# Kernel tuning notes

Measured on AMD Instinct MI355X. Metric: run time of the kernel, lower is better.

## Reference

```python
import jax, jax.numpy as jnp
import numpy as np

D_MODEL = 1024
N_HEADS = 16
D_FF = 4096
EPS = 1e-5


def setup_inputs() -> dict:
    key = jax.random.key(0)
    ks = jax.random.split(key, 13)
    d, f = D_MODEL, D_FF
    s = 1.0 / np.sqrt(d)
    sf = 1.0 / np.sqrt(f)
    return {
        "x": jax.random.normal(ks[0], (2, 2048, d), dtype=jnp.float32),
        "Wq": jax.random.normal(ks[1], (d, d), dtype=jnp.float32) * s,
        "bq": jnp.zeros((d,), jnp.float32),
        "Wk": jax.random.normal(ks[2], (d, d), dtype=jnp.float32) * s,
        "bk": jnp.zeros((d,), jnp.float32),
        "Wv": jax.random.normal(ks[3], (d, d), dtype=jnp.float32) * s,
        "bv": jnp.zeros((d,), jnp.float32),
        "Wo": jax.random.normal(ks[4], (d, d), dtype=jnp.float32) * s,
        "bo": jnp.zeros((d,), jnp.float32),
        "W1": jax.random.normal(ks[5], (f, d), dtype=jnp.float32) * s,
        "b1": jnp.zeros((f,), jnp.float32),
        "W2": jax.random.normal(ks[6], (d, f), dtype=jnp.float32) * sf,
        "b2": jnp.zeros((d,), jnp.float32),
        "g1": jnp.ones((d,), jnp.float32),
        "be1": jnp.zeros((d,), jnp.float32),
        "g2": jnp.ones((d,), jnp.float32),
        "be2": jnp.zeros((d,), jnp.float32),
    }


def _layernorm(x, g, b):
    mu = jnp.mean(x, axis=-1, keepdims=True)
    var = jnp.mean(jnp.square(x - mu), axis=-1, keepdims=True)
    return (x - mu) * jax.lax.rsqrt(var + EPS) * g + b


def reference(x, Wq, bq, Wk, bk, Wv, bv, Wo, bo, W1, b1, W2, b2, g1, be1, g2, be2):
    B, S, D = x.shape
    H = N_HEADS
    dk = D // H
    # QKV projections (torch Linear: x @ W.T + b), reshape to [B,H,S,dk]
    def proj(W, b):
        return (x @ W.T + b).reshape(B, S, H, dk).transpose(0, 2, 1, 3)
    Q, K, V = proj(Wq, bq), proj(Wk, bk), proj(Wv, bv)
    scores = jnp.einsum("bhsd,bhtd->bhst", Q, K) / jnp.sqrt(jnp.float32(dk))
    attn = jax.nn.softmax(scores, axis=-1)
    ctx = jnp.einsum("bhst,bhtd->bhsd", attn, V)
    ctx = ctx.transpose(0, 2, 1, 3).reshape(B, S, D)
    attn_out = ctx @ Wo.T + bo
    x1 = _layernorm(x + attn_out, g1, be1)
    ff = jax.nn.relu(x1 @ W1.T + b1) @ W2.T + b2
    return _layernorm(x1 + ff, g2, be2)
```

## Files before the change

kernel.cpp:

```cpp
#include <hip/hip_runtime.h>

typedef unsigned short u16;
typedef unsigned int u32;
typedef unsigned long long u64;
typedef __attribute__((ext_vector_type(8))) short short8;
typedef __attribute__((ext_vector_type(4))) float f32x4;

#define D_MODEL 1024
#define SEQ 2048
#define NH 16
#define DK 64
#define DFF 4096
#define NTOK 4096
#define LOG2E 1.44269504f

__device__ __forceinline__ u16 f2bf(float f) {
    unsigned x = __builtin_bit_cast(unsigned, f);
    x = x + 0x7fffu + ((x >> 16) & 1u);
    return (u16)(x >> 16);
}

__device__ __forceinline__ float fexp2(float x) {
    float r;
    asm("v_exp_f32 %0, %1" : "=v"(r) : "v"(x));
    return r;
}

__device__ __forceinline__ void gload_lds16(const void* g, void* l) {
    __builtin_amdgcn_global_load_lds(
        (__attribute__((address_space(1))) void*)g,
        (__attribute__((address_space(3))) void*)l, 16, 0, 0);
}

__device__ __forceinline__ void cvt_body(const float* __restrict__ in,
                                         u16* __restrict__ out, int blk) {
    size_t i = ((size_t)blk * 256 + threadIdx.x) * 4;
    float4 v = *(const float4*)(in + i);
    out[i + 0] = f2bf(v.x);
    out[i + 1] = f2bf(v.y);
    out[i + 2] = f2bf(v.z);
    out[i + 3] = f2bf(v.w);
}

__global__ __launch_bounds__(256) void cvt_bf16_x4(
    const float* __restrict__ sx, const float* __restrict__ s0,
    const float* __restrict__ s1, const float* __restrict__ s2,
    const float* __restrict__ s3, u16* __restrict__ dx, u16* __restrict__ d0,
    u16* __restrict__ d1, u16* __restrict__ d2, u16* __restrict__ d3) {
    int f = blockIdx.x;
    if (f < 4096) {
        cvt_body(sx, dx, f);
    } else {
        int which = (f - 4096) >> 10, blk = (f - 4096) & 1023;
        const float* s = which == 0 ? s0 : which == 1 ? s1 : which == 2 ? s2 : s3;
        u16* d = which == 0 ? d0 : which == 1 ? d1 : which == 2 ? d2 : d3;
        cvt_body(s, d, blk);
    }
}

__global__ __launch_bounds__(256) void cvt_bf16_2(
    const float* __restrict__ s0, const float* __restrict__ s1,
    u16* __restrict__ d0, u16* __restrict__ d1) {
    int which = blockIdx.x >> 12, blk = blockIdx.x & 4095;
    cvt_body(which ? s1 : s0, which ? d1 : d0, blk);
}

template <int BM, int BN>
__device__ __forceinline__ void gemm_acc(const u16* __restrict__ A,
                                         const u16* __restrict__ W,
                                         int K, int m0, int n0,
                                         f32x4 (&acc)[BM / 32][BN / 32]) {
    constexpr int MR = BM / 32, NR = BN / 32;
    __shared__ short8 As[2][BM / 2][8];
    __shared__ short8 Bs[2][BN / 2][8];
    const int tid = threadIdx.x;
    const int lane = tid & 63, w = tid >> 6;
    const int l15 = lane & 15, lg = lane >> 4;
    const int wr = (w >> 1) * (BM / 2), wc = (w & 1) * (BN / 2);
    const int pswA = l15 >> 1;
    const int cbase = ((l15 & 1) << 2) + lg;

#pragma unroll
    for (int i = 0; i < MR; ++i)
#pragma unroll
        for (int j = 0; j < NR; ++j) acc[i][j] = (f32x4){0.f, 0.f, 0.f, 0.f};

#define STAGE_AB(B_, K0)                                                       \
    {                                                                          \
        _Pragma("unroll") for (int j = 0; j < BM / 64; ++j) {                  \
            int idx = j * 256 + tid;                                           \
            int prow = idx >> 3;                                               \
            int s = (idx & 7) ^ (prow & 7);                                    \
            int lrow = prow * 2 + (s >> 2), lc = s & 3;                        \
            gload_lds16(A + (size_t)(m0 + lrow) * K + (K0) + lc * 8,           \
                        (char*)As[B_] + (j * 256 + w * 64) * 16);              \
        }                                                                      \
        _Pragma("unroll") for (int j = 0; j < BN / 64; ++j) {                  \
            int idx = j * 256 + tid;                                           \
            int prow = idx >> 3;                                               \
            int s = (idx & 7) ^ (prow & 7);                                    \
            int lrow = prow * 2 + (s >> 2), lc = s & 3;                        \
            gload_lds16(W + (size_t)(n0 + lrow) * K + (K0) + lc * 8,           \
                        (char*)Bs[B_] + (j * 256 + w * 64) * 16);              \
        }                                                                      \
    }
#define COMPUTE(B_)                                                            \
    {                                                                          \
        short8 af[MR], bf[NR];                                                 \
        _Pragma("unroll") for (int m = 0; m < MR; ++m)                         \
            af[m] = As[B_][(wr + m * 16) / 2 + (l15 >> 1)][cbase ^ pswA];      \
        _Pragma("unroll") for (int n = 0; n < NR; ++n)                         \
            bf[n] = Bs[B_][(wc + n * 16) / 2 + (l15 >> 1)][cbase ^ pswA];      \
        _Pragma("unroll") for (int m = 0; m < MR; ++m)                         \
            _Pragma("unroll") for (int n = 0; n < NR; ++n)                     \
                acc[m][n] = __builtin_amdgcn_mfma_f32_16x16x32_bf16(           \
                    af[m], bf[n], acc[m][n], 0, 0, 0);                         \
    }

    STAGE_AB(0, 0);
    for (int k0 = 0; k0 < K; k0 += 64) {
        __syncthreads();
        STAGE_AB(1, k0 + 32);
        COMPUTE(0);
        __syncthreads();
        if (k0 + 64 < K) STAGE_AB(0, k0 + 64);
        COMPUTE(1);
    }
#undef STAGE_AB
#undef COMPUTE
}

template <int BM, int BN, int EPI, int XCD>
__global__ __launch_bounds__(256) void gemm_bt(
    const u16* __restrict__ A, const u16* __restrict__ W,
    const float* __restrict__ bias, u16* __restrict__ outb,
    float* __restrict__ outf, int M, int N, int K) {
    int m0, n0;
    if (XCD) {
        int f = blockIdx.x;
        int xcd = f & 7, j = f >> 3;
        int mq = xcd >> 1, nh = xcd & 1;
        int mi = j & 7, ni = j >> 3;
        m0 = (mq * 8 + mi) * BM;
        n0 = (nh * 16 + ni) * BN;
    } else {
        m0 = blockIdx.y * BM;
        n0 = blockIdx.x * BN;
    }
    f32x4 acc[BM / 32][BN / 32];
    gemm_acc<BM, BN>(A, W, K, m0, n0, acc);
    const int lane = threadIdx.x & 63, w = threadIdx.x >> 6;
    const int l15 = lane & 15, lg = lane >> 4;
    const int wr = (w >> 1) * (BM / 2), wc = (w & 1) * (BN / 2);
#pragma unroll
    for (int m = 0; m < BM / 32; ++m)
#pragma unroll
        for (int n = 0; n < BN / 32; ++n) {
            int gn = n0 + wc + n * 16 + l15;
            float bv = bias[gn];
#pragma unroll
            for (int r = 0; r < 4; ++r) {
                int gm = m0 + wr + m * 16 + lg * 4 + r;
                float v = acc[m][n][r] + bv;
                if (EPI == 0) outf[(size_t)gm * N + gn] = v;
                else outb[(size_t)gm * N + gn] = f2bf(fmaxf(v, 0.f));
            }
        }
}

__global__ __launch_bounds__(256) void gemm_k64(
    const u16* __restrict__ A, const u16* __restrict__ W,
    const float* __restrict__ bias, float* __restrict__ outf,
    float* __restrict__ outf2, int M, int N, int K, int KZ) {
    __shared__ short8 As[64][8];
    __shared__ short8 Bs[128][8];
    const int tid = threadIdx.x;
    const int lane = tid & 63, w = tid >> 6;
    const int l15 = lane & 15, lg = lane >> 4;
    const int wr = (w >> 1) * 32, wc = (w & 1) * 64;
    const int psw = l15 & 7;
    const int f = blockIdx.x;
    const int xcd = f & 7, j = f >> 3;
    const int mi = j & 7, n = (j >> 3) & 7, kz = j >> 6;
    const int m0 = (xcd * 8 + mi) * 64, n0 = n * 128;
    const int kl = K / KZ, kbase = kz * kl;
    float* out = kz ? outf2 : outf;

    f32x4 acc[2][4];
#pragma unroll
    for (int i = 0; i < 2; ++i)
#pragma unroll
        for (int jj = 0; jj < 4; ++jj) acc[i][jj] = (f32x4){0.f, 0.f, 0.f, 0.f};

    for (int k0 = kbase; k0 < kbase + kl; k0 += 64) {
        __syncthreads();
#pragma unroll
        for (int jj = 0; jj < 2; ++jj) {
            int idx = jj * 256 + tid;
            int r = idx >> 3, ck = idx & 7;
            gload_lds16(A + (size_t)(m0 + r) * K + k0 + ((ck ^ (r & 7)) * 8),
                        (char*)As + (jj * 256 + w * 64) * 16);
        }
#pragma unroll
        for (int jj = 0; jj < 4; ++jj) {
            int idx = jj * 256 + tid;
            int r = idx >> 3, ck = idx & 7;
            gload_lds16(W + (size_t)(n0 + r) * K + k0 + ((ck ^ (r & 7)) * 8),
                        (char*)Bs + (jj * 256 + w * 64) * 16);
        }
        __syncthreads();

#pragma unroll
        for (int kk = 0; kk < 2; ++kk) {
            short8 af[2], bf[4];
#pragma unroll
            for (int m = 0; m < 2; ++m)
                af[m] = As[wr + m * 16 + l15][(kk * 4 + lg) ^ psw];
#pragma unroll
            for (int nn = 0; nn < 4; ++nn)
                bf[nn] = Bs[wc + nn * 16 + l15][(kk * 4 + lg) ^ psw];
#pragma unroll
            for (int m = 0; m < 2; ++m)
#pragma unroll
                for (int nn = 0; nn < 4; ++nn)
                    acc[m][nn] = __builtin_amdgcn_mfma_f32_16x16x32_bf16(
                        af[m], bf[nn], acc[m][nn], 0, 0, 0);
        }
    }

#pragma unroll
    for (int m = 0; m < 2; ++m)
#pragma unroll
        for (int nn = 0; nn < 4; ++nn) {
            int gn = n0 + wc + nn * 16 + l15;
            float bv = (kz == 0) ? bias[gn] : 0.f;
#pragma unroll
            for (int r = 0; r < 4; ++r) {
                int gm = m0 + wr + m * 16 + lg * 4 + r;
                out[(size_t)gm * N + gn] = acc[m][nn][r] + bv;
            }
        }
}

__global__ __launch_bounds__(256) void gemm_qkv(
    const u16* __restrict__ A, const u16* __restrict__ Wq,
    const u16* __restrict__ Wk, const u16* __restrict__ Wv,
    const float* __restrict__ bq, const float* __restrict__ bk,
    const float* __restrict__ bv, u16* __restrict__ Qo, u16* __restrict__ Ko,
    u16* __restrict__ Vo) {
    const int f = blockIdx.x;
    const int xcd = f & 7, j = f >> 3;
    const int mi = j & 3, q = j >> 2;
    const int mat = q >> 3;
    const int m0 = (xcd * 4 + mi) * 128, n0 = (q & 7) * 128;
    const u16* W = mat == 0 ? Wq : (mat == 1 ? Wk : Wv);
    const float* bias = mat == 0 ? bq : (mat == 1 ? bk : bv);
    const float scale = (mat == 0) ? 0.125f * LOG2E : 1.0f;
    f32x4 acc[4][4];
    gemm_acc<128, 128>(A, W, D_MODEL, m0, n0, acc);
    const int lane = threadIdx.x & 63, w = threadIdx.x >> 6;
    const int l15 = lane & 15, lg = lane >> 4;
    const int wr = (w >> 1) * 64, wc = (w & 1) * 64;

    if (mat == 2) {
#pragma unroll
        for (int m = 0; m < 4; ++m)
#pragma unroll
            for (int n = 0; n < 4; ++n) {
                int gn = n0 + wc + n * 16 + l15;
                float bv2 = bias[gn];
                int h = gn >> 6, d = gn & 63;
                int gm0 = m0 + wr + m * 16 + lg * 4;
                int b = gm0 >> 11, s = gm0 & 2047;
                u64 pk = (u64)f2bf(acc[m][n][0] + bv2) |
                         ((u64)f2bf(acc[m][n][1] + bv2) << 16) |
                         ((u64)f2bf(acc[m][n][2] + bv2) << 32) |
                         ((u64)f2bf(acc[m][n][3] + bv2) << 48);
                size_t obase = (size_t)(b * NH + h) * DK * SEQ;
                int soff = (s & ~63) + ((((s >> 3) & 7) ^ (d & 7)) << 3) + (s & 7);
                *(u64*)(Vo + obase + (size_t)d * SEQ + soff) = pk;
            }
    } else {
        u16* out = mat == 0 ? Qo : Ko;
#pragma unroll
        for (int m = 0; m < 4; ++m)
#pragma unroll
            for (int n = 0; n < 4; ++n) {
                int gn = n0 + wc + n * 16 + l15;
                float bv2 = bias[gn];
                int h = gn >> 6, d = gn & 63;
#pragma unroll
                for (int r = 0; r < 4; ++r) {
                    int gm = m0 + wr + m * 16 + lg * 4 + r;
                    int b = gm >> 11, s = gm & 2047;
                    float v = (acc[m][n][r] + bv2) * scale;
                    out[(((size_t)(b * NH + h)) * SEQ + s) * DK + d] = f2bf(v);
                }
            }
    }
}

#define KVB 64
__global__ __launch_bounds__(256) void attn_fwd(const u16* __restrict__ Q,
                                                const u16* __restrict__ Kp,
                                                const u16* __restrict__ Vg_,
                                                u16* __restrict__ ctx) {
    __shared__ __align__(16) u16 Kt[2][64 * 64];
    __shared__ __align__(16) u16 Vt[2][64 * 64];
    __shared__ __align__(16) u16 Ps[4][16 * 64];

    const int tid = threadIdx.x;
    const int lane = tid & 63;
    const int w = tid >> 6;
    const int l15 = lane & 15;
    const int lg = lane >> 4;
    const int f = blockIdx.x + 32 * blockIdx.y;
    const int bh = f & 31;
    const int qblk = f >> 5;
    const int qbase = qblk * 64 + w * 16;
    const u16* Qb = Q + (size_t)bh * SEQ * DK;
    const u16* Kb = Kp + (size_t)bh * SEQ * DK;
    const u16* Vg = Vg_ + (size_t)bh * DK * SEQ;

    short8 qf[2];
#pragma unroll
    for (int hf = 0; hf < 2; ++hf)
        qf[hf] = *(const short8*)(Qb + (size_t)(qbase + l15) * DK + hf * 32 + lg * 8);

    short8 onesf;
#pragma unroll
    for (int e = 0; e < 8; ++e) onesf[e] = (short)0x3F80;

    f32x4 zero = {0.f, 0.f, 0.f, 0.f};
    f32x4 o[4], o1 = zero;
#pragma unroll
    for (int db = 0; db < 4; ++db) o[db] = zero;
    float m_own = 0.f;

    u16* Pu = Ps[w];
    const int psw = l15 & 7;

#define STAGE_V(T0, BUF)                                                       \
    {                                                                          \
        _Pragma("unroll") for (int j = 0; j < 2; ++j) {                        \
            int idx = j * 256 + tid;                                           \
            gload_lds16(Vg + (size_t)(idx >> 3) * SEQ + (T0) + (idx & 7) * 8,  \
                        (char*)Vt[BUF] + (j * 256 + w * 64) * 16);             \
        }                                                                      \
    }
#define STAGE_K(T0, BUF)                                                       \
    {                                                                          \
        _Pragma("unroll") for (int j = 0; j < 2; ++j) {                        \
            int idx = j * 256 + tid;                                           \
            int kv = idx >> 3, ck = idx & 7;                                   \
            gload_lds16(Kb + (size_t)((T0) + kv) * DK + ((ck ^ (kv & 7)) * 8), \
                        (char*)Kt[BUF] + (j * 256 + w * 64) * 16);             \
        }                                                                      \
    }
#define KF(BUF, NB, HALF)                                                      \
    (*(const short8*)((const char*)Kt[BUF] + ((NB)*16 + l15) * 128 +           \
                      (((((HALF)*4 + lg)) ^ psw) << 4)))

#define ATTN_TILE(BUF)                                                         \
    {                                                                          \
        f32x4 seed = {-m_own, -m_own, -m_own, -m_own};                         \
        f32x4 sc[4];                                                           \
        __builtin_amdgcn_s_setprio(1);                                         \
        _Pragma("unroll") for (int nb = 0; nb < 4; ++nb) {                     \
            sc[nb] = __builtin_amdgcn_mfma_f32_16x16x32_bf16(                  \
                KF(BUF, nb, 0), qf[0], seed, 0, 0, 0);                         \
            sc[nb] = __builtin_amdgcn_mfma_f32_16x16x32_bf16(                  \
                KF(BUF, nb, 1), qf[1], sc[nb], 0, 0, 0);                       \
        }                                                                      \
        __builtin_amdgcn_s_setprio(0);                                         \
        float a0 = fmaxf(fmaxf(sc[0][0], sc[0][1]), sc[0][2]);                 \
        float a1 = fmaxf(fmaxf(sc[0][3], sc[1][0]), sc[1][1]);                 \
        float a2 = fmaxf(fmaxf(sc[1][2], sc[1][3]), sc[2][0]);                 \
        float a3 = fmaxf(fmaxf(sc[2][1], sc[2][2]), sc[2][3]);                 \
        float a4 = fmaxf(fmaxf(sc[3][0], sc[3][1]), sc[3][2]);                 \
        float lm = fmaxf(fmaxf(fmaxf(a0, a1), a2),                             \
                         fmaxf(fmaxf(a3, a4), sc[3][3]));                      \
        if (__any(lm > 8.f)) {                                                 \
            float rv = fmaxf(lm, __shfl_xor(lm, 16));                          \
            rv = fmaxf(rv, __shfl_xor(rv, 32));                                \
            float rvp = fmaxf(rv, 0.f);                                        \
            float fac = fexp2(-rvp);                                           \
            m_own += rvp;                                                      \
            _Pragma("unroll") for (int nb = 0; nb < 4; ++nb)                   \
                _Pragma("unroll") for (int r = 0; r < 4; ++r)                  \
                    sc[nb][r] -= rvp;                                          \
            _Pragma("unroll") for (int r = 0; r < 4; ++r) {                    \
                float fr = __shfl(fac, lg * 4 + r);                            \
                o1[r] *= fr;                                                   \
                _Pragma("unroll") for (int db = 0; db < 4; ++db)               \
                    o[db][r] *= fr;                                            \
            }                                                                  \
        }                                                                      \
        _Pragma("unroll") for (int nb = 0; nb < 4; ++nb) {                     \
            float p0 = fexp2(sc[nb][0]);                                       \
            float p1 = fexp2(sc[nb][1]);                                       \
            float p2 = fexp2(sc[nb][2]);                                       \
            float p3 = fexp2(sc[nb][3]);                                       \
            u32 pk01 = __builtin_amdgcn_perm(__builtin_bit_cast(u32, p1),      \
                                             __builtin_bit_cast(u32, p0),      \
                                             0x07060302u);                     \
            u32 pk23 = __builtin_amdgcn_perm(__builtin_bit_cast(u32, p3),      \
                                             __builtin_bit_cast(u32, p2),      \
                                             0x07060302u);                     \
            int ck = (nb * 2 + (lg >> 1)) ^ psw;                               \
            u64* dst = (u64*)(Pu + l15 * 64 + ck * 8 + (lg & 1) * 4);          \
            *dst = (u64)pk01 | ((u64)pk23 << 32);                              \
        }                                                                      \
        short8 pa[2];                                                          \
        _Pragma("unroll") for (int ts = 0; ts < 2; ++ts)                       \
            pa[ts] = *(const short8*)(Pu + l15 * 64 + (((ts * 4 + lg) ^ psw) * 8)); \
        __builtin_amdgcn_s_setprio(1);                                         \
        _Pragma("unroll") for (int db = 0; db < 4; ++db) {                     \
            const int d = db * 16 + l15;                                       \
            _Pragma("unroll") for (int ts = 0; ts < 2; ++ts) {                 \
                short8 vb = *(const short8*)((const char*)Vt[BUF] + d * 128 +  \
                                             (((ts * 4 + lg) ^ psw) << 4));    \
                o[db] = __builtin_amdgcn_mfma_f32_16x16x32_bf16(               \
                    pa[ts], vb, o[db], 0, 0, 0);                               \
            }                                                                  \
        }                                                                      \
        o1 = __builtin_amdgcn_mfma_f32_16x16x32_bf16(pa[0], onesf, o1, 0, 0, 0); \
        o1 = __builtin_amdgcn_mfma_f32_16x16x32_bf16(pa[1], onesf, o1, 0, 0, 0); \
        __builtin_amdgcn_s_setprio(0);                                         \
    }

    STAGE_K(0, 0);
    STAGE_V(0, 0);

    for (int t0 = 0; t0 < SEQ; t0 += 2 * KVB) {
        __syncthreads();
        STAGE_K(t0 + KVB, 1);
        STAGE_V(t0 + KVB, 1);
        ATTN_TILE(0);
        __syncthreads();
        if (t0 + 2 * KVB < SEQ) {
            STAGE_K(t0 + 2 * KVB, 0);
            STAGE_V(t0 + 2 * KVB, 0);
        }
        ATTN_TILE(1);
    }

    const int b = bh >> 4, h = bh & 15;
#pragma unroll
    for (int r = 0; r < 4; ++r) {
        float inv = 1.0f / o1[r];
        int srow = qbase + lg * 4 + r;
        size_t rowoff = ((size_t)(b * SEQ + srow)) * D_MODEL + h * DK;
#pragma unroll
        for (int db = 0; db < 4; ++db)
            ctx[rowoff + db * 16 + l15] = f2bf(o[db][r] * inv);
    }
#undef STAGE_V
#undef STAGE_K
#undef KF
#undef ATTN_TILE
}

__global__ __launch_bounds__(256) void ln_res(const float* __restrict__ X,
                                              const float* __restrict__ Y,
                                              const float* __restrict__ Y2,
                                              const float* __restrict__ gamma,
                                              const float* __restrict__ beta,
                                              float* __restrict__ outf,
                                              u16* __restrict__ outb) {
    __shared__ float red[8];
    const int row = blockIdx.x, t = threadIdx.x;
    const size_t off = (size_t)row * D_MODEL + t * 4;
    float4 xv = *(const float4*)(X + off);
    float4 yv = *(const float4*)(Y + off);
    float sx = xv.x + yv.x, sy = xv.y + yv.y, sz = xv.z + yv.z, sw = xv.w + yv.w;
    if (Y2) {
        float4 y2 = *(const float4*)(Y2 + off);
        sx += y2.x; sy += y2.y; sz += y2.z; sw += y2.w;
    }
    float ps = sx + sy + sz + sw;
#pragma unroll
    for (int o2 = 32; o2; o2 >>= 1) ps += __shfl_xor(ps, o2);
    if ((t & 63) == 0) red[t >> 6] = ps;
    __syncthreads();
    float mu = (red[0] + red[1] + red[2] + red[3]) * (1.0f / D_MODEL);
    float d0 = sx - mu, d1 = sy - mu, d2 = sz - mu, d3 = sw - mu;
    float p2 = d0 * d0 + d1 * d1 + d2 * d2 + d3 * d3;
#pragma unroll
    for (int o2 = 32; o2; o2 >>= 1) p2 += __shfl_xor(p2, o2);
    if ((t & 63) == 0) red[4 + (t >> 6)] = p2;
    __syncthreads();
    float var = (red[4] + red[5] + red[6] + red[7]) * (1.0f / D_MODEL);
    float rstd = rsqrtf(var + 1e-5f);
    float4 gv = *(const float4*)(gamma + t * 4);
    float4 bv = *(const float4*)(beta + t * 4);
    float r0 = d0 * rstd * gv.x + bv.x;
    float r1 = d1 * rstd * gv.y + bv.y;
    float r2 = d2 * rstd * gv.z + bv.z;
    float r3 = d3 * rstd * gv.w + bv.w;
    float4 res; res.x = r0; res.y = r1; res.z = r2; res.w = r3;
    *(float4*)(outf + off) = res;
    if (outb) {
        outb[off + 0] = f2bf(r0);
        outb[off + 1] = f2bf(r1);
        outb[off + 2] = f2bf(r2);
        outb[off + 3] = f2bf(r3);
    }
}

extern "C" void kernel_launch(void* const* d_in, const int* in_sizes, int n_in,
                              void* d_out, int out_size, void* d_ws, size_t ws_size,
                              hipStream_t stream) {
    (void)in_sizes; (void)n_in; (void)out_size; (void)ws_size;
    const float* x  = (const float*)d_in[0];
    const float* Wq = (const float*)d_in[1];
    const float* bq = (const float*)d_in[2];
    const float* Wk = (const float*)d_in[3];
    const float* bk = (const float*)d_in[4];
    const float* Wv = (const float*)d_in[5];
    const float* bv = (const float*)d_in[6];
    const float* Wo = (const float*)d_in[7];
    const float* bo = (const float*)d_in[8];
    const float* W1 = (const float*)d_in[9];
    const float* b1 = (const float*)d_in[10];
    const float* W2 = (const float*)d_in[11];
    const float* b2 = (const float*)d_in[12];
    const float* g1 = (const float*)d_in[13];
    const float* be1 = (const float*)d_in[14];
    const float* g2 = (const float*)d_in[15];
    const float* be2 = (const float*)d_in[16];

    char* ws = (char*)d_ws;
    u16* xb   = (u16*)(ws);
    u16* Qb   = (u16*)(ws + ((size_t)8 << 20));
    u16* Kb   = (u16*)(ws + ((size_t)16 << 20));
    u16* Vb   = (u16*)(ws + ((size_t)24 << 20));
    float* x1 = (float*)(ws + ((size_t)32 << 20));
    float* Fs = (float*)(ws + ((size_t)48 << 20));
    u16* hb   = (u16*)(ws + ((size_t)64 << 20));
    u16* Wqb = hb;
    u16* Wkb = hb + (1u << 20);
    u16* Wvb = hb + (2u << 20);
    u16* Wob = hb + (3u << 20);
    u16* W1b = Qb;
    u16* W2b = Kb;
    u16* Vtg = (u16*)Fs;
    u16* ctxb = xb;
    u16* x1b  = Vb;
    float* Fs2 = (float*)ws;

    cvt_bf16_x4<<<dim3(8192), 256, 0, stream>>>(x, Wq, Wk, Wv, Wo,
                                                xb, Wqb, Wkb, Wvb, Wob);

    gemm_qkv<<<dim3(768), 256, 0, stream>>>(xb, Wqb, Wkb, Wvb, bq, bk, bv,
                                            Qb, Kb, Vtg);

    attn_fwd<<<dim3(SEQ / 64, 32), 256, 0, stream>>>(Qb, Kb, Vtg, ctxb);

    cvt_bf16_2<<<dim3(8192), 256, 0, stream>>>(W1, W2, W1b, W2b);

    gemm_k64<<<dim3(512), 256, 0, stream>>>(ctxb, Wob, bo, Fs, nullptr,
                                            NTOK, D_MODEL, D_MODEL, 1);

    ln_res<<<dim3(NTOK), 256, 0, stream>>>(x, Fs, nullptr, g1, be1, x1, x1b);

    gemm_bt<128, 128, 1, 1><<<dim3(1024), 256, 0, stream>>>(
        x1b, W1b, b1, hb, nullptr, NTOK, DFF, D_MODEL);

    gemm_k64<<<dim3(1024), 256, 0, stream>>>(hb, W2b, b2, Fs, Fs2,
                                             NTOK, D_MODEL, DFF, 2);

    ln_res<<<dim3(NTOK), 256, 0, stream>>>(x1, Fs, Fs2, g2, be2,
                                           (float*)d_out, nullptr);
}
```

Measured before the change: 274.1 us.

## Store GEMM outputs as bf16 and widen attention blocks to 128 queries

The Wo and W2 GEMM epilogues now write bf16 instead of fp32 partial results, and the residual-LayerNorm kernels read them as bf16. This halves the write and read traffic for those intermediates, at the cost of extra rounding before the LayerNorm. The attention kernel now uses 512 threads (8 waves) per block covering 128 query rows, so each staged K/V tile is shared by twice as many waves. Each thread now issues one staging load instead of two.

Result: faster. 255.4 us (-6.8%).

```diff
diff --git a/kernel.cpp b/kernel.cpp
--- a/kernel.cpp
+++ b/kernel.cpp
@@ -18,6 +18,10 @@
     unsigned x = __builtin_bit_cast(unsigned, f);
     x = x + 0x7fffu + ((x >> 16) & 1u);
     return (u16)(x >> 16);
+}
+
+__device__ __forceinline__ float bf2f(u16 v) {
+    return __builtin_bit_cast(float, (u32)v << 16);
 }
 
 __device__ __forceinline__ float fexp2(float x) {
@@ -170,8 +174,8 @@
 
 __global__ __launch_bounds__(256) void gemm_k64(
     const u16* __restrict__ A, const u16* __restrict__ W,
-    const float* __restrict__ bias, float* __restrict__ outf,
-    float* __restrict__ outf2, int M, int N, int K, int KZ) {
+    const float* __restrict__ bias, u16* __restrict__ outb,
+    u16* __restrict__ outb2, int M, int N, int K, int KZ) {
     __shared__ short8 As[64][8];
     __shared__ short8 Bs[128][8];
     const int tid = threadIdx.x;
@@ -184,7 +188,7 @@
     const int mi = j & 7, n = (j >> 3) & 7, kz = j >> 6;
     const int m0 = (xcd * 8 + mi) * 64, n0 = n * 128;
     const int kl = K / KZ, kbase = kz * kl;
-    float* out = kz ? outf2 : outf;
+    u16* out = kz ? outb2 : outb;
 
     f32x4 acc[2][4];
 #pragma unroll
@@ -237,7 +241,7 @@
 #pragma unroll
             for (int r = 0; r < 4; ++r) {
                 int gm = m0 + wr + m * 16 + lg * 4 + r;
-                out[(size_t)gm * N + gn] = acc[m][nn][r] + bv;
+                out[(size_t)gm * N + gn] = f2bf(acc[m][nn][r] + bv);
             }
         }
 }
@@ -301,23 +305,23 @@
 }
 
 #define KVB 64
-__global__ __launch_bounds__(256) void attn_fwd(const u16* __restrict__ Q,
+__global__ __launch_bounds__(512) void attn_fwd(const u16* __restrict__ Q,
                                                 const u16* __restrict__ Kp,
                                                 const u16* __restrict__ Vg_,
                                                 u16* __restrict__ ctx) {
     __shared__ __align__(16) u16 Kt[2][64 * 64];
     __shared__ __align__(16) u16 Vt[2][64 * 64];
-    __shared__ __align__(16) u16 Ps[4][16 * 64];
+    __shared__ __align__(16) u16 Ps[8][16 * 64];
 
     const int tid = threadIdx.x;
     const int lane = tid & 63;
     const int w = tid >> 6;
     const int l15 = lane & 15;
     const int lg = lane >> 4;
-    const int f = blockIdx.x + 32 * blockIdx.y;
+    const int f = blockIdx.x + 16 * blockIdx.y;
     const int bh = f & 31;
     const int qblk = f >> 5;
-    const int qbase = qblk * 64 + w * 16;
+    const int qbase = qblk * 128 + w * 16;
     const u16* Qb = Q + (size_t)bh * SEQ * DK;
     const u16* Kb = Kp + (size_t)bh * SEQ * DK;
     const u16* Vg = Vg_ + (size_t)bh * DK * SEQ;
@@ -342,20 +346,14 @@
 
 #define STAGE_V(T0, BUF)                                                       \
     {                                                                          \
-        _Pragma("unroll") for (int j = 0; j < 2; ++j) {                        \
-            int idx = j * 256 + tid;                                           \
-            gload_lds16(Vg + (size_t)(idx >> 3) * SEQ + (T0) + (idx & 7) * 8,  \
-                        (char*)Vt[BUF] + (j * 256 + w * 64) * 16);             \
-        }                                                                      \
+        gload_lds16(Vg + (size_t)(tid >> 3) * SEQ + (T0) + (tid & 7) * 8,      \
+                    (char*)Vt[BUF] + (w * 64) * 16);                           \
     }
 #define STAGE_K(T0, BUF)                                                       \
     {                                                                          \
-        _Pragma("unroll") for (int j = 0; j < 2; ++j) {                        \
-            int idx = j * 256 + tid;                                           \
-            int kv = idx >> 3, ck = idx & 7;                                   \
-            gload_lds16(Kb + (size_t)((T0) + kv) * DK + ((ck ^ (kv & 7)) * 8), \
-                        (char*)Kt[BUF] + (j * 256 + w * 64) * 16);             \
-        }                                                                      \
+        int kv = tid >> 3, ck = tid & 7;                                       \
+        gload_lds16(Kb + (size_t)((T0) + kv) * DK + ((ck ^ (kv & 7)) * 8),     \
+                    (char*)Kt[BUF] + (w * 64) * 16);                           \
     }
 #define KF(BUF, NB, HALF)                                                      \
     (*(const short8*)((const char*)Kt[BUF] + ((NB)*16 + l15) * 128 +           \
@@ -462,8 +460,8 @@
 }
 
 __global__ __launch_bounds__(256) void ln_res(const float* __restrict__ X,
-                                              const float* __restrict__ Y,
-                                              const float* __restrict__ Y2,
+                                              const u16* __restrict__ Y,
+                                              const u16* __restrict__ Y2,
                                               const float* __restrict__ gamma,
                                               const float* __restrict__ beta,
                                               float* __restrict__ outf,
@@ -472,11 +470,12 @@
     const int row = blockIdx.x, t = threadIdx.x;
     const size_t off = (size_t)row * D_MODEL + t * 4;
     float4 xv = *(const float4*)(X + off);
-    float4 yv = *(const float4*)(Y + off);
-    float sx = xv.x + yv.x, sy = xv.y + yv.y, sz = xv.z + yv.z, sw = xv.w + yv.w;
+    ushort4 yv = *(const ushort4*)(Y + off);
+    float sx = xv.x + bf2f(yv.x), sy = xv.y + bf2f(yv.y);
+    float sz = xv.z + bf2f(yv.z), sw = xv.w + bf2f(yv.w);
     if (Y2) {
-        float4 y2 = *(const float4*)(Y2 + off);
-        sx += y2.x; sy += y2.y; sz += y2.z; sw += y2.w;
+        ushort4 y2 = *(const ushort4*)(Y2 + off);
+        sx += bf2f(y2.x); sy += bf2f(y2.y); sz += bf2f(y2.z); sw += bf2f(y2.w);
     }
     float ps = sx + sy + sz + sw;
 #pragma unroll
@@ -536,7 +535,8 @@
     u16* Kb   = (u16*)(ws + ((size_t)16 << 20));
     u16* Vb   = (u16*)(ws + ((size_t)24 << 20));
     float* x1 = (float*)(ws + ((size_t)32 << 20));
-    float* Fs = (float*)(ws + ((size_t)48 << 20));
+    u16* Fs   = (u16*)(ws + ((size_t)48 << 20));
+    u16* Fs2  = (u16*)(ws + ((size_t)56 << 20));
     u16* hb   = (u16*)(ws + ((size_t)64 << 20));
     u16* Wqb = hb;
     u16* Wkb = hb + (1u << 20);
@@ -544,10 +544,9 @@
     u16* Wob = hb + (3u << 20);
     u16* W1b = Qb;
     u16* W2b = Kb;
-    u16* Vtg = (u16*)Fs;
+    u16* Vtg = Fs;
     u16* ctxb = xb;
     u16* x1b  = Vb;
-    float* Fs2 = (float*)ws;
 
     cvt_bf16_x4<<<dim3(8192), 256, 0, stream>>>(x, Wq, Wk, Wv, Wo,
                                                 xb, Wqb, Wkb, Wvb, Wob);
@@ -555,7 +554,7 @@
     gemm_qkv<<<dim3(768), 256, 0, stream>>>(xb, Wqb, Wkb, Wvb, bq, bk, bv,
                                             Qb, Kb, Vtg);
 
-    attn_fwd<<<dim3(SEQ / 64, 32), 256, 0, stream>>>(Qb, Kb, Vtg, ctxb);
+    attn_fwd<<<dim3(SEQ / 128, 32), 512, 0, stream>>>(Qb, Kb, Vtg, ctxb);
 
     cvt_bf16_2<<<dim3(8192), 256, 0, stream>>>(W1, W2, W1b, W2b);
 
```
